# Performance work log

Hardware: AMD Instinct MI355X
Metric: run time of the kernel (lower is better)

## Reference

```python
import jax, jax.numpy as jnp
import numpy as np

TEMPERATURE = 0.07
NEG_INF = -9e15
EPS = 1e-12

def setup_inputs() -> dict:
    key = jax.random.key(0)
    k1, k2 = jax.random.split(key)
    N, D = 8192, 128
    features = jax.random.normal(k1, (N, D), dtype=jnp.float32)
    labels = jax.random.randint(k2, (N,), 0, 16, dtype=jnp.int64)
    return {"features": features, "labels": labels}

def reference(features, labels):
    N = features.shape[0]
    # L2 normalize rows (torch F.normalize: x / max(||x||, eps))
    norm = jnp.linalg.norm(features, axis=1, keepdims=True)
    f = features / jnp.maximum(norm, EPS)
    # [N, N] similarity
    sim = jnp.matmul(f, f.T) / TEMPERATURE
    eye = jnp.eye(N, dtype=bool)
    sim = jnp.where(eye, NEG_INF, sim)
    # positive-pair mask: same label, excluding self
    pos_mask = ((labels[:, None] == labels[None, :]) & ~eye).astype(sim.dtype)
    denom = jnp.exp(sim).sum(axis=1, keepdims=True)  # [N, 1]
    log_prob = sim - jnp.log(denom + EPS)
    loss = -(pos_mask * log_prob).sum(axis=1) / (pos_mask.sum(axis=1) + EPS)
    return loss.mean()
```

## Files before the change

kernel.cpp:

```cpp
#include <hip/hip_runtime.h>
#include <hip/hip_bf16.h>

#define EPS 1e-12f
#define SQRT_C_EXP 4.53981597f
#define M_LN2F 0.69314718056f
#define NUM_CLASSES 16
#define CS_BLOCKS 128

#define BM 128
#define BN 64
#define KD 128
#define NCHUNK 16
#define NCOLG 8
#define NPART 32

typedef __attribute__((ext_vector_type(4))) float f32x4;
typedef __attribute__((ext_vector_type(8))) short bf16x8;

__device__ __forceinline__ float bf2f(ushort u) {
    unsigned int x = ((unsigned int)u) << 16;
    return __uint_as_float(x);
}

__device__ __forceinline__ void gload16(const void* g, void* l) {
    __builtin_amdgcn_global_load_lds(
        (const __attribute__((address_space(1))) void*)g,
        (__attribute__((address_space(3))) void*)l, 16, 0, 0);
}

__device__ __forceinline__ const bf16x8* lds_frag(const ushort* base, int r, int slot) {
    int sw = slot ^ (r & 7);
    return reinterpret_cast<const bf16x8*>(
        reinterpret_cast<const char*>(base) + r * 256 + sw * 16);
}

__global__ void normalize_kernel(const float* __restrict__ feat,
                                 ushort* __restrict__ fb,
                                 float* __restrict__ sq,
                                 float* __restrict__ gz,
                                 int N) {
    if (blockIdx.x == 0) {
        for (int i = threadIdx.x; i < NUM_CLASSES * KD + NUM_CLASSES; i += 256)
            gz[i] = 0.f;
    }
    int r    = (blockIdx.x * blockDim.x + threadIdx.x) >> 6;
    int lane = threadIdx.x & 63;
    if (r >= N) return;
    const float2 v = *reinterpret_cast<const float2*>(feat + (size_t)r * KD + lane * 2);
    float s = v.x * v.x + v.y * v.y;
    #pragma unroll
    for (int off = 1; off < 64; off <<= 1) s += __shfl_xor(s, off);
    const float scale = SQRT_C_EXP / fmaxf(sqrtf(s), EPS);

    __hip_bfloat16 h0 = __float2bfloat16(v.x * scale);
    __hip_bfloat16 h1 = __float2bfloat16(v.y * scale);
    ushort u0 = *reinterpret_cast<ushort*>(&h0);
    ushort u1 = *reinterpret_cast<ushort*>(&h1);
    unsigned int pack = (unsigned int)u0 | ((unsigned int)u1 << 16);
    *reinterpret_cast<unsigned int*>(fb + (size_t)r * KD + lane * 2) = pack;

    float q0 = bf2f(u0), q1 = bf2f(u1);
    float q = q0 * q0 + q1 * q1;
    #pragma unroll
    for (int off = 1; off < 64; off <<= 1) q += __shfl_xor(q, off);
    if (lane == 0) sq[r] = q;
}

__global__ __launch_bounds__(256) void classsum_kernel(
    const ushort* __restrict__ fb,
    const int* __restrict__ labels,
    float* __restrict__ g,
    float* __restrict__ cntf,
    int N) {
    __shared__ float lds[2][NUM_CLASSES][128];
    __shared__ float ldc[2][NUM_CLASSES];
    const int d    = threadIdx.x & 127;
    const int half = threadIdx.x >> 7;
    #pragma unroll
    for (int c = 0; c < NUM_CLASSES; c++) lds[half][c][d] = 0.f;
    if (d < NUM_CLASSES) ldc[half][d] = 0.f;
    __syncthreads();

    const int r0 = blockIdx.x * 64 + half * 32;
    for (int r = r0; r < r0 + 32; r++) {
        int lab = labels[r];
        lds[half][lab][d] += bf2f(fb[(size_t)r * KD + d]);
        if (d == 0) ldc[half][lab] += 1.f;
    }
    __syncthreads();

    for (int c = half; c < NUM_CLASSES; c += 2)
        atomicAdd(&g[c * KD + d], lds[0][c][d] + lds[1][c][d]);
    if (threadIdx.x < NUM_CLASSES)
        atomicAdd(&cntf[threadIdx.x], ldc[0][threadIdx.x] + ldc[1][threadIdx.x]);
}

__global__ __launch_bounds__(512, 4) void supcon_denom(
    const ushort* __restrict__ fb,
    float* __restrict__ denom_part,
    int N) {

    __shared__ __align__(16) ushort As[BM * KD];
    __shared__ __align__(16) ushort Bs[2][BN * KD];

    const int tid  = threadIdx.x;
    const int lane = tid & 63;
    const int w    = tid >> 6;
    const int wr   = w >> 2;
    const int wc   = w & 3;
    const int r16  = lane & 15;
    const int g4   = lane >> 4;

    const int rowbase = blockIdx.y * BM;
    const int col0    = blockIdx.x * (BN * NCHUNK);

    {
        const ushort* gA = fb + (size_t)rowbase * KD;
        #pragma unroll
        for (int i = 0; i < 4; i++) {
            int d = i * 512 + tid;
            int s = d ^ ((d >> 4) & 7);
            gload16(gA + (size_t)s * 8, &As[d * 8]);
        }
        const ushort* gB = fb + (size_t)col0 * KD;
        #pragma unroll
        for (int i = 0; i < 2; i++) {
            int d = i * 512 + tid;
            int s = d ^ ((d >> 4) & 7);
            gload16(gB + (size_t)s * 8, &Bs[0][d * 8]);
        }
    }
    __syncthreads();

    bf16x8 a[4][4];
    #pragma unroll
    for (int ks = 0; ks < 4; ks++) {
        const int slot = ks * 4 + g4;
        #pragma unroll
        for (int m = 0; m < 4; m++)
            a[ks][m] = *lds_frag(As, wr * 64 + m * 16 + r16, slot);
    }

    float pd[4][4];
    #pragma unroll
    for (int m = 0; m < 4; m++)
        #pragma unroll
        for (int i = 0; i < 4; i++) pd[m][i] = 0.f;

    int cur = 0;
    for (int c = 0; c < NCHUNK; c++) {
        if (c + 1 < NCHUNK) {
            const ushort* gB = fb + (size_t)(col0 + (c + 1) * BN) * KD;
            ushort* dstb = Bs[cur ^ 1];
            #pragma unroll
            for (int i = 0; i < 2; i++) {
                int d = i * 512 + tid;
                int s = d ^ ((d >> 4) & 7);
                gload16(gB + (size_t)s * 8, &dstb[d * 8]);
            }
        }

        f32x4 acc[4];
        #pragma unroll
        for (int m = 0; m < 4; m++) acc[m] = f32x4{0.f, 0.f, 0.f, 0.f};

        const ushort* bbase = Bs[cur];
        #pragma unroll
        for (int ks = 0; ks < 4; ks++) {
            const int slot = ks * 4 + g4;
            bf16x8 bv = *lds_frag(bbase, wc * 16 + r16, slot);
            #pragma unroll
            for (int m = 0; m < 4; m++)
                acc[m] = __builtin_amdgcn_mfma_f32_16x16x32_bf16(a[ks][m], bv, acc[m], 0, 0, 0);
        }

        #pragma unroll
        for (int m = 0; m < 4; m++)
            #pragma unroll
            for (int i = 0; i < 4; i++)
                pd[m][i] += __builtin_amdgcn_exp2f(acc[m][i]);

        __syncthreads();
        cur ^= 1;
    }

    #pragma unroll
    for (int off = 1; off < 16; off <<= 1)
        #pragma unroll
        for (int m = 0; m < 4; m++)
            #pragma unroll
            for (int i = 0; i < 4; i++)
                pd[m][i] += __shfl_xor(pd[m][i], off);

    if (r16 == 0) {
        const int part = blockIdx.x * 4 + wc;
        #pragma unroll
        for (int m = 0; m < 4; m++)
            #pragma unroll
            for (int i = 0; i < 4; i++) {
                int r = rowbase + wr * 64 + m * 16 + g4 * 4 + i;
                denom_part[(size_t)r * NPART + part] = pd[m][i];
            }
    }
}

__global__ void rowloss_kernel(const ushort* __restrict__ fb,
                               const int* __restrict__ labels,
                               const float* __restrict__ denom_part,
                               const float* __restrict__ sq,
                               const float* __restrict__ g,
                               const float* __restrict__ cntf,
                               float* __restrict__ rowloss,
                               int N) {
    int r    = (blockIdx.x * blockDim.x + threadIdx.x) >> 6;
    int lane = threadIdx.x & 63;
    if (r >= N) return;
    int lab = labels[r];
    unsigned int pk = *reinterpret_cast<const unsigned int*>(fb + (size_t)r * KD + lane * 2);
    float f0 = bf2f((ushort)(pk & 0xffff));
    float f1 = bf2f((ushort)(pk >> 16));
    const float2 gv = *reinterpret_cast<const float2*>(g + lab * KD + lane * 2);
    float p = f0 * gv.x + f1 * gv.y;
    #pragma unroll
    for (int off = 1; off < 64; off <<= 1) p += __shfl_xor(p, off);

    float dsum = (lane < NPART) ? denom_part[(size_t)r * NPART + lane] : 0.f;
    #pragma unroll
    for (int off = 1; off < NPART; off <<= 1) dsum += __shfl_xor(dsum, off);

    if (lane == 0) {
        float sqr    = sq[r];
        float possum = (p - sqr) * M_LN2F;
        float cnt    = cntf[lab] - 1.0f;
        float dn     = dsum - __builtin_amdgcn_exp2f(sqr);
        rowloss[r]   = -(possum - cnt * logf(dn + EPS)) / (cnt + EPS);
    }
}

__global__ void reduce_kernel(const float* __restrict__ rowloss,
                              float* __restrict__ out, int N) {
    __shared__ float sdata[16];
    float s = 0.f;
    for (int r = threadIdx.x; r < N; r += blockDim.x) s += rowloss[r];
    #pragma unroll
    for (int off = 1; off < 64; off <<= 1) s += __shfl_xor(s, off);
    int wv = threadIdx.x >> 6;
    if ((threadIdx.x & 63) == 0) sdata[wv] = s;
    __syncthreads();
    if (threadIdx.x == 0) {
        float t = 0.f;
        int nw = (int)(blockDim.x >> 6);
        for (int i = 0; i < nw; i++) t += sdata[i];
        out[0] = t / (float)N;
    }
}

extern "C" void kernel_launch(void* const* d_in, const int* in_sizes, int n_in,
                              void* d_out, int out_size, void* d_ws, size_t ws_size,
                              hipStream_t stream) {
    const float* feat = (const float*)d_in[0];
    const int* labels = (const int*)d_in[1];
    const int N = in_sizes[1];

    char* ws = (char*)d_ws;
    size_t off = 0;
    ushort* fb = (ushort*)(ws + off);                 off += (size_t)N * KD * sizeof(ushort);
    float* g     = (float*)(ws + off);                off += (size_t)NUM_CLASSES * KD * sizeof(float);
    float* cntf  = (float*)(ws + off);                off += (size_t)NUM_CLASSES * sizeof(float);
    float* sq         = (float*)(ws + off);           off += (size_t)N * sizeof(float);
    float* denom_part = (float*)(ws + off);           off += (size_t)N * NPART * sizeof(float);
    float* rowloss    = (float*)(ws + off);

    normalize_kernel<<<(N + 3) / 4, 256, 0, stream>>>(feat, fb, sq, g, N);
    classsum_kernel<<<CS_BLOCKS, 256, 0, stream>>>(fb, labels, g, cntf, N);

    dim3 grid(NCOLG, N / BM);
    supcon_denom<<<grid, 512, 0, stream>>>(fb, denom_part, N);

    rowloss_kernel<<<(N + 3) / 4, 256, 0, stream>>>(fb, labels, denom_part, sq, g, cntf, rowloss, N);
    reduce_kernel<<<1, 1024, 0, stream>>>(rowloss, (float*)d_out, N);
}
```

Before: 50.66 us.

## Exploit similarity symmetry: compute upper-triangular tiles with row and column exp sums

Replaces the full N×N denominator sweep with a triangular tiling over 256×256 blocks. Each off-diagonal block contributes both row sums and column sums of exp(sim), which roughly halves the MFMA and exp work. Partial sums are stored column-major per tile index and reduced in rowloss. It raises LDS use to two full 256-row tiles and drops double buffering, which lowers occupancy. It also adds a serial tile-index decode loop and a load imbalance on diagonal blocks.

```diff
diff --git a/kernel.cpp b/kernel.cpp
--- a/kernel.cpp
+++ b/kernel.cpp
@@ -7,11 +7,9 @@
 #define NUM_CLASSES 16
 #define CS_BLOCKS 128
 
-#define BM 128
-#define BN 64
 #define KD 128
-#define NCHUNK 16
-#define NCOLG 8
+#define TT 32
+#define NBLK (TT*(TT+1)/2)
 #define NPART 32
 
 typedef __attribute__((ext_vector_type(4))) float f32x4;
@@ -95,42 +93,49 @@
         atomicAdd(&cntf[threadIdx.x], ldc[0][threadIdx.x] + ldc[1][threadIdx.x]);
 }
 
-__global__ __launch_bounds__(512, 4) void supcon_denom(
+__global__ __launch_bounds__(512, 2) void supcon_symdenom(
     const ushort* __restrict__ fb,
-    float* __restrict__ denom_part,
+    float* __restrict__ part,
     int N) {
 
-    __shared__ __align__(16) ushort As[BM * KD];
-    __shared__ __align__(16) ushort Bs[2][BN * KD];
+    __shared__ __align__(16) ushort As[256 * KD];
+    __shared__ __align__(16) ushort Bs[256 * KD];
+    __shared__ float rowbuf[2][256];
+    __shared__ float colbuf[4][256];
 
     const int tid  = threadIdx.x;
     const int lane = tid & 63;
     const int w    = tid >> 6;
-    const int wr   = w >> 2;
-    const int wc   = w & 3;
+    const int wr   = w >> 1;
+    const int wc   = w & 1;
     const int r16  = lane & 15;
     const int g4   = lane >> 4;
 
-    const int rowbase = blockIdx.y * BM;
-    const int col0    = blockIdx.x * (BN * NCHUNK);
+    int I = 0, rem = blockIdx.x;
+    while (rem >= TT - I) { rem -= TT - I; I++; }
+    const int J = I + rem;
 
     {
-        const ushort* gA = fb + (size_t)rowbase * KD;
-        #pragma unroll
-        for (int i = 0; i < 4; i++) {
+        const ushort* gA = fb + (size_t)(I * 256) * KD;
+        #pragma unroll
+        for (int i = 0; i < 8; i++) {
             int d = i * 512 + tid;
             int s = d ^ ((d >> 4) & 7);
             gload16(gA + (size_t)s * 8, &As[d * 8]);
         }
-        const ushort* gB = fb + (size_t)col0 * KD;
-        #pragma unroll
-        for (int i = 0; i < 2; i++) {
-            int d = i * 512 + tid;
-            int s = d ^ ((d >> 4) & 7);
-            gload16(gB + (size_t)s * 8, &Bs[0][d * 8]);
+        if (J != I) {
+            const ushort* gB = fb + (size_t)(J * 256) * KD;
+            #pragma unroll
+            for (int i = 0; i < 8; i++) {
+                int d = i * 512 + tid;
+                int s = d ^ ((d >> 4) & 7);
+                gload16(gB + (size_t)s * 8, &Bs[d * 8]);
+            }
         }
     }
     __syncthreads();
+
+    const ushort* bbase = (J == I) ? As : Bs;
 
     bf16x8 a[4][4];
     #pragma unroll
@@ -147,41 +152,34 @@
         #pragma unroll
         for (int i = 0; i < 4; i++) pd[m][i] = 0.f;
 
-    int cur = 0;
-    for (int c = 0; c < NCHUNK; c++) {
-        if (c + 1 < NCHUNK) {
-            const ushort* gB = fb + (size_t)(col0 + (c + 1) * BN) * KD;
-            ushort* dstb = Bs[cur ^ 1];
-            #pragma unroll
-            for (int i = 0; i < 2; i++) {
-                int d = i * 512 + tid;
-                int s = d ^ ((d >> 4) & 7);
-                gload16(gB + (size_t)s * 8, &dstb[d * 8]);
-            }
-        }
+    #pragma unroll 1
+    for (int n = 0; n < 8; n++) {
+        const int crow = wc * 128 + n * 16 + r16;
 
         f32x4 acc[4];
         #pragma unroll
         for (int m = 0; m < 4; m++) acc[m] = f32x4{0.f, 0.f, 0.f, 0.f};
 
-        const ushort* bbase = Bs[cur];
         #pragma unroll
         for (int ks = 0; ks < 4; ks++) {
-            const int slot = ks * 4 + g4;
-            bf16x8 bv = *lds_frag(bbase, wc * 16 + r16, slot);
+            bf16x8 bv = *lds_frag(bbase, crow, ks * 4 + g4);
             #pragma unroll
             for (int m = 0; m < 4; m++)
                 acc[m] = __builtin_amdgcn_mfma_f32_16x16x32_bf16(a[ks][m], bv, acc[m], 0, 0, 0);
         }
 
-        #pragma unroll
-        for (int m = 0; m < 4; m++)
-            #pragma unroll
-            for (int i = 0; i < 4; i++)
-                pd[m][i] += __builtin_amdgcn_exp2f(acc[m][i]);
-
-        __syncthreads();
-        cur ^= 1;
+        float cs = 0.f;
+        #pragma unroll
+        for (int m = 0; m < 4; m++)
+            #pragma unroll
+            for (int i = 0; i < 4; i++) {
+                const float e = __builtin_amdgcn_exp2f(acc[m][i]);
+                pd[m][i] += e;
+                cs += e;
+            }
+        cs += __shfl_xor(cs, 16);
+        cs += __shfl_xor(cs, 32);
+        if (g4 == 0) colbuf[wr][crow] = cs;
     }
 
     #pragma unroll
@@ -193,20 +191,27 @@
                 pd[m][i] += __shfl_xor(pd[m][i], off);
 
     if (r16 == 0) {
-        const int part = blockIdx.x * 4 + wc;
-        #pragma unroll
-        for (int m = 0; m < 4; m++)
-            #pragma unroll
-            for (int i = 0; i < 4; i++) {
-                int r = rowbase + wr * 64 + m * 16 + g4 * 4 + i;
-                denom_part[(size_t)r * NPART + part] = pd[m][i];
-            }
+        #pragma unroll
+        for (int m = 0; m < 4; m++)
+            #pragma unroll
+            for (int i = 0; i < 4; i++)
+                rowbuf[wc][wr * 64 + m * 16 + g4 * 4 + i] = pd[m][i];
+    }
+    __syncthreads();
+
+    if (tid < 256) {
+        float rs = rowbuf[0][tid] + rowbuf[1][tid];
+        part[(size_t)J * N + I * 256 + tid] = rs;
+    } else if (J > I) {
+        int c = tid - 256;
+        float csum = colbuf[0][c] + colbuf[1][c] + colbuf[2][c] + colbuf[3][c];
+        part[(size_t)I * N + J * 256 + c] = csum;
     }
 }
 
 __global__ void rowloss_kernel(const ushort* __restrict__ fb,
                                const int* __restrict__ labels,
-                               const float* __restrict__ denom_part,
+                               const float* __restrict__ part,
                                const float* __restrict__ sq,
                                const float* __restrict__ g,
                                const float* __restrict__ cntf,
@@ -224,7 +229,7 @@
     #pragma unroll
     for (int off = 1; off < 64; off <<= 1) p += __shfl_xor(p, off);
 
-    float dsum = (lane < NPART) ? denom_part[(size_t)r * NPART + lane] : 0.f;
+    float dsum = (lane < NPART) ? part[(size_t)lane * N + r] : 0.f;
     #pragma unroll
     for (int off = 1; off < NPART; off <<= 1) dsum += __shfl_xor(dsum, off);
 
@@ -267,16 +272,15 @@
     ushort* fb = (ushort*)(ws + off);                 off += (size_t)N * KD * sizeof(ushort);
     float* g     = (float*)(ws + off);                off += (size_t)NUM_CLASSES * KD * sizeof(float);
     float* cntf  = (float*)(ws + off);                off += (size_t)NUM_CLASSES * sizeof(float);
-    float* sq         = (float*)(ws + off);           off += (size_t)N * sizeof(float);
-    float* denom_part = (float*)(ws + off);           off += (size_t)N * NPART * sizeof(float);
-    float* rowloss    = (float*)(ws + off);
+    float* sq      = (float*)(ws + off);              off += (size_t)N * sizeof(float);
+    float* part    = (float*)(ws + off);              off += (size_t)NPART * N * sizeof(float);
+    float* rowloss = (float*)(ws + off);
 
     normalize_kernel<<<(N + 3) / 4, 256, 0, stream>>>(feat, fb, sq, g, N);
     classsum_kernel<<<CS_BLOCKS, 256, 0, stream>>>(fb, labels, g, cntf, N);
 
-    dim3 grid(NCOLG, N / BM);
-    supcon_denom<<<grid, 512, 0, stream>>>(fb, denom_part, N);
-
-    rowloss_kernel<<<(N + 3) / 4, 256, 0, stream>>>(fb, labels, denom_part, sq, g, cntf, rowloss, N);
+    supcon_symdenom<<<NBLK, 512, 0, stream>>>(fb, part, N);
+
+    rowloss_kernel<<<(N + 3) / 4, 256, 0, stream>>>(fb, labels, part, sq, g, cntf, rowloss, N);
     reduce_kernel<<<1, 1024, 0, stream>>>(rowloss, (float*)d_out, N);
 }
```

Result: slower. 55.96 us (+10.5%).
